# Kernel tuning notes

Measured on AMD Instinct MI355X. Metric: run time of the kernel, lower is better.

The kernel has to match this reference:

```python
import jax, jax.numpy as jnp
import numpy as np

N_NODES = 50000


def _cluster_gcn_conv(x, row, col, W_out, b_out, W_root, num_nodes):
    # PyG ClusterGCNConv with diag_lambda=0.0 and self-loops already added.
    deg = jax.ops.segment_sum(jnp.ones_like(col, dtype=x.dtype), col,
                              num_segments=num_nodes)
    deg_inv = 1.0 / jnp.clip(deg, 1.0)
    w = deg_inv[col]                       # [E_total]
    msg = x[row] * w[:, None]              # [E_total, d] gather + scale
    agg = jax.ops.segment_sum(msg, col, num_segments=num_nodes)  # scatter-add
    return agg @ W_out + b_out + x @ W_root


def setup_inputs() -> dict:
    key = jax.random.key(0)
    ks = jax.random.split(key, 12)
    N, E, d_in, d_h, d_out = N_NODES, 800000, 128, 128, 64
    x = jax.random.normal(ks[0], (N, d_in), dtype=jnp.float32)
    edge_index = jax.random.randint(ks[1], (2, E), 0, N, dtype=jnp.int64)
    s = lambda fan_in: 1.0 / np.sqrt(fan_in)
    return {
        "x": x,
        "edge_index": edge_index,
        "W1_out": jax.random.normal(ks[2], (d_in, d_h), jnp.float32) * s(d_in),
        "b1": jnp.zeros((d_h,), jnp.float32),
        "W1_root": jax.random.normal(ks[3], (d_in, d_h), jnp.float32) * s(d_in),
        "W2_out": jax.random.normal(ks[4], (d_h, d_h), jnp.float32) * s(d_h),
        "b2": jnp.zeros((d_h,), jnp.float32),
        "W2_root": jax.random.normal(ks[5], (d_h, d_h), jnp.float32) * s(d_h),
        "W3_out": jax.random.normal(ks[6], (d_h, d_out), jnp.float32) * s(d_h),
        "b3": jnp.zeros((d_out,), jnp.float32),
        "W3_root": jax.random.normal(ks[7], (d_h, d_out), jnp.float32) * s(d_h),
    }


def reference(x, edge_index, W1_out, b1, W1_root, W2_out, b2, W2_root,
              W3_out, b3, W3_root):
    N = x.shape[0]
    loops = jnp.arange(N, dtype=edge_index.dtype)
    row = jnp.concatenate([edge_index[0], loops])  # add self loops
    col = jnp.concatenate([edge_index[1], loops])
    # layer 1 + relu (dropout is identity at inference)
    x = jax.nn.relu(_cluster_gcn_conv(x, row, col, W1_out, b1, W1_root, N))
    # layer 2 + relu
    x = jax.nn.relu(_cluster_gcn_conv(x, row, col, W2_out, b2, W2_root, N))
    # layer 3 + relu, then log_softmax (no pooling: node classification)
    x = jax.nn.relu(_cluster_gcn_conv(x, row, col, W3_out, b3, W3_root, N))
    return jax.nn.log_softmax(x, axis=-1)
```

## Files before the change

kernel.cpp:

```cpp
#include <hip/hip_runtime.h>
#include <math.h>


constexpr int DK = 128;
constexpr int NBUCK = 256;

typedef __attribute__((ext_vector_type(8))) short bf16x8;
typedef __attribute__((ext_vector_type(4))) float f32x4;

__device__ inline unsigned short f2bf(float f) {
    unsigned int u; __builtin_memcpy(&u, &f, 4);
    unsigned int r = (u + 0x7FFFu + ((u >> 16) & 1u)) >> 16;
    return (unsigned short)r;
}
__device__ inline float blo(unsigned int u) {
    unsigned int t = u << 16; float f; __builtin_memcpy(&f, &t, 4); return f;
}
__device__ inline float bhi(unsigned int u) {
    unsigned int t = u & 0xffff0000u; float f; __builtin_memcpy(&f, &t, 4); return f;
}

__device__ void wprep_body(const float* __restrict__ Wout, const float* __restrict__ Wroot,
                           uint4* __restrict__ frag, int dout, int tid) {
    int total = 8 * (dout >> 4) * 64;
    if (tid >= total) return;
    int L = tid & 63;
    int fu = (tid >> 6) % (dout >> 4);
    int t = (tid >> 6) / (dout >> 4);
    int quad = L >> 4, l15 = L & 15;
    int n = fu * 16 + l15;
    unsigned int p[4];
#pragma unroll
    for (int jj = 0; jj < 4; ++jj) {
        int k0 = t * 32 + quad * 8 + jj * 2;
        float v0 = (k0 < 128) ? Wout[k0 * dout + n] : Wroot[(k0 - 128) * dout + n];
        int k1 = k0 + 1;
        float v1 = (k1 < 128) ? Wout[k1 * dout + n] : Wroot[(k1 - 128) * dout + n];
        p[jj] = (unsigned)f2bf(v0) | ((unsigned)f2bf(v1) << 16);
    }
    frag[tid] = make_uint4(p[0], p[1], p[2], p[3]);
}

__global__ void k_prep(const float4* __restrict__ x, uint2* __restrict__ xb,
                       int* __restrict__ bhist, const int* __restrict__ col,
                       int n4, int E, int bspan,
                       const float* __restrict__ W1o, const float* __restrict__ W1r, uint4* wf1,
                       const float* __restrict__ W2o, const float* __restrict__ W2r, uint4* wf2,
                       const float* __restrict__ W3o, const float* __restrict__ W3r, uint4* wf3) {
    const int nxblk = (n4 + 255) / 256;
    const int b = blockIdx.x;
    const int tid = threadIdx.x;
    if (b < nxblk) {
        int i = b * 256 + tid;
        if (i >= n4) return;
        float4 v = x[i];
        uint2 o;
        o.x = (unsigned)f2bf(v.x) | ((unsigned)f2bf(v.y) << 16);
        o.y = (unsigned)f2bf(v.z) | ((unsigned)f2bf(v.w) << 16);
        xb[i] = o;
    } else if (b < nxblk + 16) {
        wprep_body(W1o, W1r, wf1, 128, (b - nxblk) * 256 + tid);
    } else if (b < nxblk + 32) {
        wprep_body(W2o, W2r, wf2, 128, (b - nxblk - 16) * 256 + tid);
    } else if (b < nxblk + 40) {
        wprep_body(W3o, W3r, wf3, 64, (b - nxblk - 32) * 256 + tid);
    } else {
        __shared__ int h[NBUCK];
        h[tid] = 0;
        __syncthreads();
        for (int i = (b - nxblk - 40) * 256 + tid; i < E; i += 400 * 256)
            atomicAdd(&h[col[i] / bspan], 1);
        __syncthreads();
        int v = h[tid];
        if (v) atomicAdd(&bhist[tid], v);
    }
}

__global__ void k_bscan(const int* __restrict__ bhist, int* __restrict__ boffs,
                        int* __restrict__ bcur, int* __restrict__ offs,
                        int n, int e) {
    __shared__ int wsum[4];
    const int tid = threadIdx.x, lane = tid & 63, wid = tid >> 6;
    int v = bhist[tid];
    int ps = v;
#pragma unroll
    for (int off = 1; off < 64; off <<= 1) {
        int t = __shfl_up(ps, off);
        if (lane >= off) ps += t;
    }
    if (lane == 63) wsum[wid] = ps;
    __syncthreads();
    int wb = 0;
    for (int w = 0; w < wid; ++w) wb += wsum[w];
    int excl = wb + ps - v;
    boffs[tid] = excl;
    bcur[tid] = excl;
    if (tid == 255) boffs[256] = excl + v;
    if (tid == 0) offs[n] = e;
}

__global__ void k_part(const int* __restrict__ row, const int* __restrict__ col,
                       int* __restrict__ bcur, unsigned int* __restrict__ ebuf,
                       int e, int bspan) {
    __shared__ int cnt[NBUCK];
    __shared__ int base[NBUCK];
    const int tid = threadIdx.x;
    const int t0 = blockIdx.x * 4096;
    cnt[tid] = 0;
    __syncthreads();
    int bk[16];
#pragma unroll
    for (int k = 0; k < 16; ++k) {
        int i = t0 + k * 256 + tid;
        int b = -1;
        if (i < e) { b = col[i] / bspan; atomicAdd(&cnt[b], 1); }
        bk[k] = b;
    }
    __syncthreads();
    base[tid] = cnt[tid] ? atomicAdd(&bcur[tid], cnt[tid]) : 0;
    cnt[tid] = 0;
    __syncthreads();
#pragma unroll
    for (int k = 0; k < 16; ++k) {
        int i = t0 + k * 256 + tid;
        if (i < e) {
            int b = bk[k];
            int slot = base[b] + atomicAdd(&cnt[b], 1);
            unsigned int colofs = (unsigned)(col[i] - b * bspan);
            ebuf[slot] = ((unsigned)row[i] & 0xFFFFu) | (colofs << 16);
        }
    }
}

__global__ void k_fillb(const unsigned int* __restrict__ ebuf,
                        const int* __restrict__ boffs, int* __restrict__ offs,
                        float* __restrict__ deginv, unsigned short* __restrict__ srow,
                        int n, int bspan) {
    __shared__ int cnt[4096];
    __shared__ int wsum[4];
    const int b = blockIdx.x, tid = threadIdx.x;
    const int start = boffs[b], end = boffs[b + 1];
    for (int i = tid; i < 4096; i += 256) cnt[i] = 0;
    __syncthreads();
    for (int i = start + tid; i < end; i += 256) {
        const unsigned u = ebuf[i];
        atomicAdd(&cnt[(int)(u >> 16) * 16 + (int)((u & 0xFFFFu) >> 12)], 1);
    }
    __syncthreads();
    int v[16], s = 0;
#pragma unroll
    for (int r = 0; r < 16; ++r) { v[r] = cnt[tid * 16 + r]; s += v[r]; }
    const int lane = tid & 63, wid = tid >> 6;
    int ps = s;
#pragma unroll
    for (int off = 1; off < 64; off <<= 1) {
        int t = __shfl_up(ps, off);
        if (lane >= off) ps += t;
    }
    if (lane == 63) wsum[wid] = ps;
    __syncthreads();
    int wb = 0;
    for (int w = 0; w < wid; ++w) wb += wsum[w];
    int excl = start + wb + ps - s;
    const int node = b * bspan + tid;
    if (tid < bspan && node < n) {
        offs[node] = excl;
        deginv[node] = 1.0f / (float)(s + 1);
    }
#pragma unroll
    for (int r = 0; r < 16; ++r) { int t = v[r]; cnt[tid * 16 + r] = excl; excl += t; }
    __syncthreads();
    for (int i = start + tid; i < end; i += 256) {
        const unsigned u = ebuf[i];
        const int pos = atomicAdd(&cnt[(int)(u >> 16) * 16 + (int)((u & 0xFFFFu) >> 12)], 1);
        srow[pos] = (unsigned short)(u & 0xFFFFu);
    }
}

__global__ __launch_bounds__(256, 5)
void k_fused(const unsigned short* __restrict__ xb,
             const int* __restrict__ offs, const unsigned short* __restrict__ srow,
             const float* __restrict__ deginv,
             const uint4* __restrict__ wfrag, const float* __restrict__ bvec,
             unsigned short* __restrict__ y, int n) {
    __shared__ unsigned short At[32][136];
    const int tid = threadIdx.x;
    const int m0 = blockIdx.x * 32;
    const uint4* __restrict__ xb4 = (const uint4*)xb;

#pragma unroll
    for (int rnd = 0; rnd < 2; ++rnd) {
        const int nl = rnd * 16 + (tid >> 4);
        const int lane = tid & 15;
        const int node = m0 + nl;
        if (node < n) {
            const size_t rb = (size_t)node * 16 + lane;
            uint4 sv = xb4[rb];
            float a0 = blo(sv.x), a1 = bhi(sv.x), a2 = blo(sv.y), a3 = bhi(sv.y);
            float a4 = blo(sv.z), a5 = bhi(sv.z), a6 = blo(sv.w), a7 = bhi(sv.w);
            const int s = offs[node], e = offs[node + 1];
            int p = s;
            for (; p + 4 <= e; p += 4) {
                const int r0 = srow[p], r1 = srow[p + 1];
                const int r2 = srow[p + 2], r3 = srow[p + 3];
                const uint4 v0 = xb4[(size_t)r0 * 16 + lane];
                const uint4 v1 = xb4[(size_t)r1 * 16 + lane];
                const uint4 v2 = xb4[(size_t)r2 * 16 + lane];
                const uint4 v3 = xb4[(size_t)r3 * 16 + lane];
                a0 += (blo(v0.x) + blo(v1.x)) + (blo(v2.x) + blo(v3.x));
                a1 += (bhi(v0.x) + bhi(v1.x)) + (bhi(v2.x) + bhi(v3.x));
                a2 += (blo(v0.y) + blo(v1.y)) + (blo(v2.y) + blo(v3.y));
                a3 += (bhi(v0.y) + bhi(v1.y)) + (bhi(v2.y) + bhi(v3.y));
                a4 += (blo(v0.z) + blo(v1.z)) + (blo(v2.z) + blo(v3.z));
                a5 += (bhi(v0.z) + bhi(v1.z)) + (bhi(v2.z) + bhi(v3.z));
                a6 += (blo(v0.w) + blo(v1.w)) + (blo(v2.w) + blo(v3.w));
                a7 += (bhi(v0.w) + bhi(v1.w)) + (bhi(v2.w) + bhi(v3.w));
            }
            for (; p < e; ++p) {
                const uint4 v = xb4[(size_t)srow[p] * 16 + lane];
                a0 += blo(v.x); a1 += bhi(v.x); a2 += blo(v.y); a3 += bhi(v.y);
                a4 += blo(v.z); a5 += bhi(v.z); a6 += blo(v.w); a7 += bhi(v.w);
            }
            const float w = deginv[node];
            uint4 o;
            o.x = (unsigned)f2bf(a0 * w) | ((unsigned)f2bf(a1 * w) << 16);
            o.y = (unsigned)f2bf(a2 * w) | ((unsigned)f2bf(a3 * w) << 16);
            o.z = (unsigned)f2bf(a4 * w) | ((unsigned)f2bf(a5 * w) << 16);
            o.w = (unsigned)f2bf(a6 * w) | ((unsigned)f2bf(a7 * w) << 16);
            *(uint4*)&At[nl][lane * 8] = o;
        }
    }
    __syncthreads();

    const int w = tid >> 6, L = tid & 63;
    const int quad = L >> 4, l15 = L & 15;

    f32x4 acc[2][2];
#pragma unroll
    for (int mt = 0; mt < 2; ++mt)
#pragma unroll
        for (int u = 0; u < 2; ++u)
            acc[mt][u] = (f32x4){0.f, 0.f, 0.f, 0.f};

    const bf16x8 zf = {0, 0, 0, 0, 0, 0, 0, 0};
#pragma unroll
    for (int t = 0; t < 8; ++t) {
        bf16x8 bfr[2];
#pragma unroll
        for (int u = 0; u < 2; ++u)
            bfr[u] = *(const bf16x8*)&wfrag[(size_t)((t * 8 + (w * 2 + u)) * 64 + L)];
        const int koff = (t & 3) * 32 + quad * 8;
        bf16x8 af[2];
#pragma unroll
        for (int mt = 0; mt < 2; ++mt) {
            const int rl = mt * 16 + l15;
            if (t < 4) {
                af[mt] = *(const bf16x8*)&At[rl][koff];
            } else {
                const int r = m0 + rl;
                af[mt] = (r < n) ? *(const bf16x8*)(xb + (size_t)r * 128 + koff) : zf;
            }
        }
#pragma unroll
        for (int mt = 0; mt < 2; ++mt)
#pragma unroll
            for (int u = 0; u < 2; ++u)
                acc[mt][u] = __builtin_amdgcn_mfma_f32_16x16x32_bf16(
                    af[mt], bfr[u], acc[mt][u], 0, 0, 0);
    }

    float bb[2];
    bb[0] = bvec[w * 32 + l15];
    bb[1] = bvec[w * 32 + 16 + l15];
#pragma unroll
    for (int mt = 0; mt < 2; ++mt)
#pragma unroll
        for (int u = 0; u < 2; ++u)
#pragma unroll
            for (int r4 = 0; r4 < 4; ++r4) {
                const int r = m0 + mt * 16 + quad * 4 + r4;
                if (r < n) {
                    float v = fmaxf(acc[mt][u][r4] + bb[u], 0.f);
                    y[(size_t)r * 128 + w * 32 + u * 16 + l15] = f2bf(v);
                }
            }
}

__global__ __launch_bounds__(256, 3)
void k_gemm3hr(const unsigned short* __restrict__ xb,
               const uint4* __restrict__ wfrag, const float* __restrict__ bvec,
               unsigned short* __restrict__ H, float* __restrict__ R, int n) {
    const int tid = threadIdx.x;
    const int w = tid >> 6, L = tid & 63;
    const int quad = L >> 4, l15 = L & 15;
    const int m0 = blockIdx.x * 64;

    bf16x8 bo[4], br[4];
#pragma unroll
    for (int t = 0; t < 4; ++t) {
        bo[t] = *(const bf16x8*)&wfrag[(size_t)((t * 4 + w) * 64 + L)];
        br[t] = *(const bf16x8*)&wfrag[(size_t)(((t + 4) * 4 + w) * 64 + L)];
    }

    f32x4 accH[4], accR[4];
#pragma unroll
    for (int mt = 0; mt < 4; ++mt) {
        accH[mt] = (f32x4){0.f, 0.f, 0.f, 0.f};
        accR[mt] = (f32x4){0.f, 0.f, 0.f, 0.f};
    }

    const bf16x8 zf = {0, 0, 0, 0, 0, 0, 0, 0};
#pragma unroll
    for (int t = 0; t < 4; ++t) {
        const int koff = t * 32 + quad * 8;
        bf16x8 af[4];
#pragma unroll
        for (int mt = 0; mt < 4; ++mt) {
            const int r = m0 + mt * 16 + l15;
            af[mt] = (r < n) ? *(const bf16x8*)(xb + (size_t)r * 128 + koff) : zf;
        }
#pragma unroll
        for (int mt = 0; mt < 4; ++mt) {
            accH[mt] = __builtin_amdgcn_mfma_f32_16x16x32_bf16(af[mt], bo[t], accH[mt], 0, 0, 0);
            accR[mt] = __builtin_amdgcn_mfma_f32_16x16x32_bf16(af[mt], br[t], accR[mt], 0, 0, 0);
        }
    }

    const float bb = bvec[w * 16 + l15];
#pragma unroll
    for (int mt = 0; mt < 4; ++mt)
#pragma unroll
        for (int r4 = 0; r4 < 4; ++r4) {
            const int r = m0 + mt * 16 + quad * 4 + r4;
            if (r < n) {
                H[(size_t)r * 64 + w * 16 + l15] = f2bf(accH[mt][r4]);
                R[(size_t)r * 64 + w * 16 + l15] = accR[mt][r4] + bb;
            }
        }
}

__global__ __launch_bounds__(256, 8)
void k_gather3(const uint2* __restrict__ Hb, const float4* __restrict__ R4,
               const int* __restrict__ offs, const unsigned short* __restrict__ srow,
               const float* __restrict__ deginv, float4* __restrict__ out, int n) {
    const int node = blockIdx.x * 16 + (threadIdx.x >> 4);
    const int lane = threadIdx.x & 15;
    if (node >= n) return;
    const size_t rb = (size_t)node * 16 + lane;
    uint2 sv = Hb[rb];
    float a0 = blo(sv.x), a1 = bhi(sv.x), a2 = blo(sv.y), a3 = bhi(sv.y);
    const int s = offs[node], e = offs[node + 1];
    int p = s;
    for (; p + 4 <= e; p += 4) {
        const int r0 = srow[p], r1 = srow[p + 1], r2 = srow[p + 2], r3 = srow[p + 3];
        const uint2 v0 = Hb[(size_t)r0 * 16 + lane];
        const uint2 v1 = Hb[(size_t)r1 * 16 + lane];
        const uint2 v2 = Hb[(size_t)r2 * 16 + lane];
        const uint2 v3 = Hb[(size_t)r3 * 16 + lane];
        a0 += (blo(v0.x) + blo(v1.x)) + (blo(v2.x) + blo(v3.x));
        a1 += (bhi(v0.x) + bhi(v1.x)) + (bhi(v2.x) + bhi(v3.x));
        a2 += (blo(v0.y) + blo(v1.y)) + (blo(v2.y) + blo(v3.y));
        a3 += (bhi(v0.y) + bhi(v1.y)) + (bhi(v2.y) + bhi(v3.y));
    }
    for (; p < e; ++p) {
        const uint2 v = Hb[(size_t)srow[p] * 16 + lane];
        a0 += blo(v.x); a1 += bhi(v.x); a2 += blo(v.y); a3 += bhi(v.y);
    }
    const float w = deginv[node];
    const float4 r = R4[rb];
    float v0 = fmaxf(a0 * w + r.x, 0.f);
    float v1 = fmaxf(a1 * w + r.y, 0.f);
    float v2 = fmaxf(a2 * w + r.z, 0.f);
    float v3 = fmaxf(a3 * w + r.w, 0.f);
    float m = fmaxf(fmaxf(v0, v1), fmaxf(v2, v3));
    m = fmaxf(m, __shfl_xor(m, 1));
    m = fmaxf(m, __shfl_xor(m, 2));
    m = fmaxf(m, __shfl_xor(m, 4));
    m = fmaxf(m, __shfl_xor(m, 8));
    float s2 = __expf(v0 - m) + __expf(v1 - m) + __expf(v2 - m) + __expf(v3 - m);
    s2 += __shfl_xor(s2, 1);
    s2 += __shfl_xor(s2, 2);
    s2 += __shfl_xor(s2, 4);
    s2 += __shfl_xor(s2, 8);
    const float lse = m + __logf(s2);
    out[rb] = make_float4(v0 - lse, v1 - lse, v2 - lse, v3 - lse);
}

extern "C" void kernel_launch(void* const* d_in, const int* in_sizes, int n_in,
                              void* d_out, int out_size, void* d_ws, size_t ws_size,
                              hipStream_t stream) {
    const float* x   = (const float*)d_in[0];
    const int*   ei  = (const int*)d_in[1];
    const float* W1o = (const float*)d_in[2];
    const float* b1  = (const float*)d_in[3];
    const float* W1r = (const float*)d_in[4];
    const float* W2o = (const float*)d_in[5];
    const float* b2  = (const float*)d_in[6];
    const float* W2r = (const float*)d_in[7];
    const float* W3o = (const float*)d_in[8];
    const float* b3  = (const float*)d_in[9];
    const float* W3r = (const float*)d_in[10];

    const int N = in_sizes[0] / DK;
    const int E = in_sizes[1] / 2;
    const int* row = ei;
    const int* col = ei + E;
    const int bspan = (N + NBUCK - 1) / NBUCK;

    int*   bhist  = (int*)d_ws;
    int*   boffs  = bhist + 256;
    int*   bcur   = boffs + 288;
    int*   offs   = bcur + 256;
    float* deginv = (float*)(offs + ((N + 64) & ~63));
    unsigned short* srow = (unsigned short*)(deginv + ((N + 63) & ~63));
    unsigned int* ebuf = (unsigned int*)(srow + ((E + 63) & ~63));
    uint4* wf1    = (uint4*)(ebuf + ((E + 63) & ~63));
    uint4* wf2    = wf1 + 4096;
    uint4* wf3    = wf2 + 4096;
    unsigned short* xbuf = (unsigned short*)(wf3 + 2048);
    unsigned short* Ya   = xbuf + (size_t)N * 128;
    unsigned short* Yb   = Ya + (size_t)N * 128;
    float* out = (float*)d_out;

    const int n4 = N * 32;
    const int nxblk = (n4 + 255) / 256;

    hipMemsetAsync(bhist, 0, NBUCK * sizeof(int), stream);
    k_prep<<<nxblk + 440, 256, 0, stream>>>((const float4*)x, (uint2*)xbuf, bhist, col,
                                            n4, E, bspan,
                                            W1o, W1r, wf1, W2o, W2r, wf2, W3o, W3r, wf3);

    k_bscan<<<1, 256, 0, stream>>>(bhist, boffs, bcur, offs, N, E);
    k_part<<<(E + 4095) / 4096, 256, 0, stream>>>(row, col, bcur, ebuf, E, bspan);
    k_fillb<<<NBUCK, 256, 0, stream>>>(ebuf, boffs, offs, deginv, srow, N, bspan);

    const int Gf = (N + 31) / 32;
    const int Gg3 = (N + 15) / 16;
    const int Gm = (N + 63) / 64;

    k_fused<<<Gf, 256, 0, stream>>>(xbuf, offs, srow, deginv, wf1, b1, Ya, N);
    k_fused<<<Gf, 256, 0, stream>>>(Ya, offs, srow, deginv, wf2, b2, Yb, N);
    k_gemm3hr<<<Gm, 256, 0, stream>>>(Yb, wf3, b3, xbuf, (float*)Ya, N);
    k_gather3<<<Gg3, 256, 0, stream>>>((const uint2*)xbuf, (const float4*)Ya,
                                       offs, srow, deginv, (float4*)out, N);
}
```

Baseline: 246.6 us.

## Fuse layer-3 GEMM into layer-2 kernel and fold bucket scan into consumers

```diff
diff --git a/kernel.cpp b/kernel.cpp
--- a/kernel.cpp
+++ b/kernel.cpp
@@ -76,9 +76,11 @@
     }
 }
 
-__global__ void k_bscan(const int* __restrict__ bhist, int* __restrict__ boffs,
-                        int* __restrict__ bcur, int* __restrict__ offs,
-                        int n, int e) {
+__global__ void k_part(const int* __restrict__ row, const int* __restrict__ col,
+                       const int* __restrict__ bhist, int* __restrict__ bcur0,
+                       unsigned int* __restrict__ ebuf, int e, int bspan) {
+    __shared__ int cnt[NBUCK];
+    __shared__ int base[NBUCK];
     __shared__ int wsum[4];
     const int tid = threadIdx.x, lane = tid & 63, wid = tid >> 6;
     int v = bhist[tid];
@@ -92,19 +94,8 @@
     __syncthreads();
     int wb = 0;
     for (int w = 0; w < wid; ++w) wb += wsum[w];
-    int excl = wb + ps - v;
-    boffs[tid] = excl;
-    bcur[tid] = excl;
-    if (tid == 255) boffs[256] = excl + v;
-    if (tid == 0) offs[n] = e;
-}
-
-__global__ void k_part(const int* __restrict__ row, const int* __restrict__ col,
-                       int* __restrict__ bcur, unsigned int* __restrict__ ebuf,
-                       int e, int bspan) {
-    __shared__ int cnt[NBUCK];
-    __shared__ int base[NBUCK];
-    const int tid = threadIdx.x;
+    const int excl = wb + ps - v;
+
     const int t0 = blockIdx.x * 4096;
     cnt[tid] = 0;
     __syncthreads();
@@ -117,7 +108,7 @@
         bk[k] = b;
     }
     __syncthreads();
-    base[tid] = cnt[tid] ? atomicAdd(&bcur[tid], cnt[tid]) : 0;
+    base[tid] = excl + (cnt[tid] ? atomicAdd(&bcur0[tid], cnt[tid]) : 0);
     cnt[tid] = 0;
     __syncthreads();
 #pragma unroll
@@ -133,15 +124,34 @@
 }
 
 __global__ void k_fillb(const unsigned int* __restrict__ ebuf,
-                        const int* __restrict__ boffs, int* __restrict__ offs,
+                        const int* __restrict__ bhist, int* __restrict__ offs,
                         float* __restrict__ deginv, unsigned short* __restrict__ srow,
-                        int n, int bspan) {
+                        int n, int e, int bspan) {
     __shared__ int cnt[4096];
+    __shared__ int scan_s[NBUCK + 1];
     __shared__ int wsum[4];
     const int b = blockIdx.x, tid = threadIdx.x;
-    const int start = boffs[b], end = boffs[b + 1];
+    const int lane = tid & 63, wid = tid >> 6;
+    {
+        int v = bhist[tid];
+        int ps = v;
+#pragma unroll
+        for (int off = 1; off < 64; off <<= 1) {
+            int t = __shfl_up(ps, off);
+            if (lane >= off) ps += t;
+        }
+        if (lane == 63) wsum[wid] = ps;
+        __syncthreads();
+        int wb = 0;
+        for (int w = 0; w < wid; ++w) wb += wsum[w];
+        int excl = wb + ps - v;
+        scan_s[tid] = excl;
+        if (tid == 255) scan_s[256] = excl + v;
+    }
     for (int i = tid; i < 4096; i += 256) cnt[i] = 0;
     __syncthreads();
+    const int start = scan_s[b], end = scan_s[b + 1];
+    if (b == NBUCK - 1 && tid == 0) offs[n] = e;
     for (int i = start + tid; i < end; i += 256) {
         const unsigned u = ebuf[i];
         atomicAdd(&cnt[(int)(u >> 16) * 16 + (int)((u & 0xFFFFu) >> 12)], 1);
@@ -150,7 +160,6 @@
     int v[16], s = 0;
 #pragma unroll
     for (int r = 0; r < 16; ++r) { v[r] = cnt[tid * 16 + r]; s += v[r]; }
-    const int lane = tid & 63, wid = tid >> 6;
     int ps = s;
 #pragma unroll
     for (int off = 1; off < 64; off <<= 1) {
@@ -177,12 +186,15 @@
     }
 }
 
+template <bool HR>
 __global__ __launch_bounds__(256, 5)
 void k_fused(const unsigned short* __restrict__ xb,
              const int* __restrict__ offs, const unsigned short* __restrict__ srow,
              const float* __restrict__ deginv,
              const uint4* __restrict__ wfrag, const float* __restrict__ bvec,
-             unsigned short* __restrict__ y, int n) {
+             unsigned short* __restrict__ y,
+             const uint4* __restrict__ wfrag3, const float* __restrict__ b3,
+             unsigned short* __restrict__ H, float* __restrict__ R, int n) {
     __shared__ unsigned short At[32][136];
     const int tid = threadIdx.x;
     const int m0 = blockIdx.x * 32;
@@ -272,69 +284,66 @@
     float bb[2];
     bb[0] = bvec[w * 32 + l15];
     bb[1] = bvec[w * 32 + 16 + l15];
+
+    if (!HR) {
+#pragma unroll
+        for (int mt = 0; mt < 2; ++mt)
+#pragma unroll
+            for (int u = 0; u < 2; ++u)
+#pragma unroll
+                for (int r4 = 0; r4 < 4; ++r4) {
+                    const int r = m0 + mt * 16 + quad * 4 + r4;
+                    if (r < n) {
+                        float v = fmaxf(acc[mt][u][r4] + bb[u], 0.f);
+                        y[(size_t)r * 128 + w * 32 + u * 16 + l15] = f2bf(v);
+                    }
+                }
+        return;
+    }
+
+    __syncthreads();
 #pragma unroll
     for (int mt = 0; mt < 2; ++mt)
 #pragma unroll
         for (int u = 0; u < 2; ++u)
 #pragma unroll
             for (int r4 = 0; r4 < 4; ++r4) {
-                const int r = m0 + mt * 16 + quad * 4 + r4;
-                if (r < n) {
-                    float v = fmaxf(acc[mt][u][r4] + bb[u], 0.f);
-                    y[(size_t)r * 128 + w * 32 + u * 16 + l15] = f2bf(v);
-                }
+                const int rl = mt * 16 + quad * 4 + r4;
+                float v = fmaxf(acc[mt][u][r4] + bb[u], 0.f);
+                At[rl][w * 32 + u * 16 + l15] = f2bf(v);
             }
-}
-
-__global__ __launch_bounds__(256, 3)
-void k_gemm3hr(const unsigned short* __restrict__ xb,
-               const uint4* __restrict__ wfrag, const float* __restrict__ bvec,
-               unsigned short* __restrict__ H, float* __restrict__ R, int n) {
-    const int tid = threadIdx.x;
-    const int w = tid >> 6, L = tid & 63;
-    const int quad = L >> 4, l15 = L & 15;
-    const int m0 = blockIdx.x * 64;
-
-    bf16x8 bo[4], br[4];
-#pragma unroll
-    for (int t = 0; t < 4; ++t) {
-        bo[t] = *(const bf16x8*)&wfrag[(size_t)((t * 4 + w) * 64 + L)];
-        br[t] = *(const bf16x8*)&wfrag[(size_t)(((t + 4) * 4 + w) * 64 + L)];
-    }
-
-    f32x4 accH[4], accR[4];
-#pragma unroll
-    for (int mt = 0; mt < 4; ++mt) {
+    __syncthreads();
+
+    f32x4 accH[2], accR[2];
+#pragma unroll
+    for (int mt = 0; mt < 2; ++mt) {
         accH[mt] = (f32x4){0.f, 0.f, 0.f, 0.f};
         accR[mt] = (f32x4){0.f, 0.f, 0.f, 0.f};
     }
-
-    const bf16x8 zf = {0, 0, 0, 0, 0, 0, 0, 0};
 #pragma unroll
     for (int t = 0; t < 4; ++t) {
+        const bf16x8 bo = *(const bf16x8*)&wfrag3[(size_t)((t * 4 + w) * 64 + L)];
+        const bf16x8 br = *(const bf16x8*)&wfrag3[(size_t)(((t + 4) * 4 + w) * 64 + L)];
         const int koff = t * 32 + quad * 8;
-        bf16x8 af[4];
-#pragma unroll
-        for (int mt = 0; mt < 4; ++mt) {
-            const int r = m0 + mt * 16 + l15;
-            af[mt] = (r < n) ? *(const bf16x8*)(xb + (size_t)r * 128 + koff) : zf;
-        }
-#pragma unroll
-        for (int mt = 0; mt < 4; ++mt) {
-            accH[mt] = __builtin_amdgcn_mfma_f32_16x16x32_bf16(af[mt], bo[t], accH[mt], 0, 0, 0);
-            accR[mt] = __builtin_amdgcn_mfma_f32_16x16x32_bf16(af[mt], br[t], accR[mt], 0, 0, 0);
-        }
-    }
-
-    const float bb = bvec[w * 16 + l15];
-#pragma unroll
-    for (int mt = 0; mt < 4; ++mt)
+        bf16x8 af[2];
+#pragma unroll
+        for (int mt = 0; mt < 2; ++mt)
+            af[mt] = *(const bf16x8*)&At[mt * 16 + l15][koff];
+#pragma unroll
+        for (int mt = 0; mt < 2; ++mt) {
+            accH[mt] = __builtin_amdgcn_mfma_f32_16x16x32_bf16(af[mt], bo, accH[mt], 0, 0, 0);
+            accR[mt] = __builtin_amdgcn_mfma_f32_16x16x32_bf16(af[mt], br, accR[mt], 0, 0, 0);
+        }
+    }
+    const float bb3 = b3[w * 16 + l15];
+#pragma unroll
+    for (int mt = 0; mt < 2; ++mt)
 #pragma unroll
         for (int r4 = 0; r4 < 4; ++r4) {
             const int r = m0 + mt * 16 + quad * 4 + r4;
             if (r < n) {
                 H[(size_t)r * 64 + w * 16 + l15] = f2bf(accH[mt][r4]);
-                R[(size_t)r * 64 + w * 16 + l15] = accR[mt][r4] + bb;
+                R[(size_t)r * 64 + w * 16 + l15] = accR[mt][r4] + bb3;
             }
         }
 }
@@ -408,9 +417,8 @@
     const int bspan = (N + NBUCK - 1) / NBUCK;
 
     int*   bhist  = (int*)d_ws;
-    int*   boffs  = bhist + 256;
-    int*   bcur   = boffs + 288;
-    int*   offs   = bcur + 256;
+    int*   bcur0  = bhist + 256;
+    int*   offs   = bcur0 + 256;
     float* deginv = (float*)(offs + ((N + 64) & ~63));
     unsigned short* srow = (unsigned short*)(deginv + ((N + 63) & ~63));
     unsigned int* ebuf = (unsigned int*)(srow + ((E + 63) & ~63));
@@ -419,28 +427,28 @@
     uint4* wf3    = wf2 + 4096;
     unsigned short* xbuf = (unsigned short*)(wf3 + 2048);
     unsigned short* Ya   = xbuf + (size_t)N * 128;
-    unsigned short* Yb   = Ya + (size_t)N * 128;
+    unsigned short* Hb   = Ya + (size_t)N * 128;
+    float* Rb = (float*)(Hb + (size_t)N * 64);
     float* out = (float*)d_out;
 
     const int n4 = N * 32;
     const int nxblk = (n4 + 255) / 256;
 
-    hipMemsetAsync(bhist, 0, NBUCK * sizeof(int), stream);
+    hipMemsetAsync(bhist, 0, 512 * sizeof(int), stream);
     k_prep<<<nxblk + 440, 256, 0, stream>>>((const float4*)x, (uint2*)xbuf, bhist, col,
                                             n4, E, bspan,
                                             W1o, W1r, wf1, W2o, W2r, wf2, W3o, W3r, wf3);
 
-    k_bscan<<<1, 256, 0, stream>>>(bhist, boffs, bcur, offs, N, E);
-    k_part<<<(E + 4095) / 4096, 256, 0, stream>>>(row, col, bcur, ebuf, E, bspan);
-    k_fillb<<<NBUCK, 256, 0, stream>>>(ebuf, boffs, offs, deginv, srow, N, bspan);
+    k_part<<<(E + 4095) / 4096, 256, 0, stream>>>(row, col, bhist, bcur0, ebuf, E, bspan);
+    k_fillb<<<NBUCK, 256, 0, stream>>>(ebuf, bhist, offs, deginv, srow, N, E, bspan);
 
     const int Gf = (N + 31) / 32;
     const int Gg3 = (N + 15) / 16;
-    const int Gm = (N + 63) / 64;
-
-    k_fused<<<Gf, 256, 0, stream>>>(xbuf, offs, srow, deginv, wf1, b1, Ya, N);
-    k_fused<<<Gf, 256, 0, stream>>>(Ya, offs, srow, deginv, wf2, b2, Yb, N);
-    k_gemm3hr<<<Gm, 256, 0, stream>>>(Yb, wf3, b3, xbuf, (float*)Ya, N);
-    k_gather3<<<Gg3, 256, 0, stream>>>((const uint2*)xbuf, (const float4*)Ya,
+
+    k_fused<false><<<Gf, 256, 0, stream>>>(xbuf, offs, srow, deginv, wf1, b1, Ya,
+                                           nullptr, nullptr, nullptr, nullptr, N);
+    k_fused<true><<<Gf, 256, 0, stream>>>(Ya, offs, srow, deginv, wf2, b2, nullptr,
+                                          wf3, b3, Hb, Rb, N);
+    k_gather3<<<Gg3, 256, 0, stream>>>((const uint2*)Hb, (const float4*)Rb,
                                        offs, srow, deginv, (float4*)out, N);
 }
```

Result: faster. 229.3 us (-7.0%).
